# Kernel tuning notes

Measured on AMD Instinct MI355X. Metric: run time of the kernel, lower is better.

The kernel has to match this reference:

```python
import jax, jax.numpy as jnp
import numpy as np

N_NODES = 100000
N_EDGES = 800000
IN_FEAT = 128
HID = 128
OUT = 2


def setup_inputs() -> dict:
    key = jax.random.key(0)
    ks = jax.random.split(key, 8)
    h = jax.random.normal(ks[0], (N_NODES, IN_FEAT), dtype=jnp.float32)
    src = jax.random.randint(ks[1], (N_EDGES,), 0, N_NODES, dtype=jnp.int64)
    dst = jax.random.randint(ks[2], (N_EDGES,), 0, N_NODES, dtype=jnp.int64)
    # Linear weights stored as (fan_in, fan_out); scaled like torch's default init
    W1 = jax.random.normal(ks[3], (2 * IN_FEAT, HID), dtype=jnp.float32) / np.sqrt(2 * IN_FEAT)
    b1 = jnp.zeros((HID,), dtype=jnp.float32)
    W2 = jax.random.normal(ks[4], (HID, HID), dtype=jnp.float32) / np.sqrt(HID)
    b2 = jnp.zeros((HID,), dtype=jnp.float32)
    W3 = jax.random.normal(ks[5], (HID, OUT), dtype=jnp.float32) / np.sqrt(HID)
    b3 = jnp.zeros((OUT,), dtype=jnp.float32)
    return {"h": h, "src": src, "dst": dst,
            "W1": W1, "b1": b1, "W2": W2, "b2": b2, "W3": W3, "b3": b3}


def reference(h, src, dst, W1, b1, W2, b2, W3, b3):
    # Per-edge gather of endpoint features, concat, 3-layer MLP with ReLU
    h_u = h[src]                       # [E, F]
    h_v = h[dst]                       # [E, F]
    x = jnp.concatenate([h_u, h_v], axis=1)   # [E, 2F]
    x = jax.nn.relu(x @ W1 + b1)       # [E, HID]
    x = jax.nn.relu(x @ W2 + b2)       # [E, HID]
    score = x @ W3 + b3                # [E, OUT]
    return score
```

## Files before the change

kernel.cpp:

```cpp
#include <hip/hip_runtime.h>
#include <hip/hip_fp16.h>


typedef _Float16 half8 __attribute__((ext_vector_type(8)));
typedef _Float16 half4_t __attribute__((ext_vector_type(4)));
typedef float    f32x4 __attribute__((ext_vector_type(4)));

#define MFMA16(a, b, c) __builtin_amdgcn_mfma_f32_16x16x32_f16((a), (b), (c), 0, 0, 0)

#define N_NODES_C 100000
#define N_EDGES_C 800000

#define W1PF_OFF  0
#define W1QF_OFF  32768
#define W2F_OFF_N 65536
#define W3F_OFF_N 98304
#define P16_OFF   131072
#define TBL_HALVES (N_NODES_C * 128)
#define Q16_OFF   (P16_OFF + TBL_HALVES * 2)
#define WS_NEED_NEW ((size_t)Q16_OFF + (size_t)TBL_HALVES * 2)

#define ET 32
#define NT_E (N_EDGES_C / ET)
#define GRID_E 1024
#define NT_N ((N_NODES_C + 63) / 64)


__global__ void pack_w_new(const float* __restrict__ W1, const float* __restrict__ W2,
                           const float* __restrict__ W3, char* __restrict__ wsb) {
    int i = blockIdx.x * blockDim.x + threadIdx.x;
    _Float16* w1pf = (_Float16*)(wsb + W1PF_OFF);
    _Float16* w1qf = (_Float16*)(wsb + W1QF_OFF);
    _Float16* w2f  = (_Float16*)(wsb + W2F_OFF_N);
    _Float16* w3f  = (_Float16*)(wsb + W3F_OFF_N);
    if (i < 16384) {
        int j = i & 7, lane = (i >> 3) & 63, kk = (i >> 9) & 3, cm = i >> 11;
        int g = lane >> 4, rr = lane & 15;
        int k = 32 * kk + 8 * g + j, n = 16 * cm + rr;
        w1pf[i] = (_Float16)W1[k * 128 + n];
        w1qf[i] = (_Float16)W1[(k + 128) * 128 + n];
        w2f[i]  = (_Float16)W2[k * 128 + n];
    }
    if (i < 2048) {
        int j = i & 7, lane = (i >> 3) & 63, t = i >> 9;
        int g = lane >> 4, rr = lane & 15;
        int k = 32 * t + 4 * g + (j & 3) + 16 * (j >> 2);
        w3f[i] = (rr < 2) ? (_Float16)W3[k * 2 + rr] : (_Float16)0.0f;
    }
}

__global__ __launch_bounds__(512, 4) void pq_kernel(const float* __restrict__ h,
                                                    const float* __restrict__ b1,
                                                    char* __restrict__ wsb) {
    __shared__ float4 Htile[64 * 32];
    const int tid = threadIdx.x;
    const int w = tid >> 6, l = tid & 63, g = l >> 4, rr = l & 15;
    const int t = w >> 2, cmq = w & 3;
    const half8* wf = (const half8*)(wsb + (t ? W1QF_OFF : W1PF_OFF));
    half8 W1F[2][4];
#pragma unroll
    for (int cm = 0; cm < 2; ++cm)
#pragma unroll
        for (int kk = 0; kk < 4; ++kk)
            W1F[cm][kk] = wf[((2 * cmq + cm) * 4 + kk) * 64 + l];
    f32x4 b1v[2] = {{0.f, 0.f, 0.f, 0.f}, {0.f, 0.f, 0.f, 0.f}};
    if (t == 1) {
#pragma unroll
        for (int cm = 0; cm < 2; ++cm)
            b1v[cm] = *(const f32x4*)(b1 + 16 * (2 * cmq + cm) + 4 * g);
    }
    _Float16* tbl = (_Float16*)(wsb + (t ? Q16_OFF : P16_OFF));

    const int tile = blockIdx.x;
    const int slot = l & 31, rhalf = l >> 5;
    float4 sv[4];
    int rows[4];
#pragma unroll
    for (int i = 0; i < 4; ++i) {
        int row = 8 * w + 2 * i + rhalf;
        rows[i] = row;
        int node = tile * 64 + row;
        if (node > N_NODES_C - 1) node = N_NODES_C - 1;
        sv[i] = *(const float4*)(h + (size_t)node * 128 + slot * 4);
    }
#pragma unroll
    for (int i = 0; i < 4; ++i)
        Htile[rows[i] * 32 + (slot ^ (rows[i] & 15))] = sv[i];
    __syncthreads();

    f32x4 acc[2][4];
#pragma unroll
    for (int cm = 0; cm < 2; ++cm)
#pragma unroll
        for (int ce = 0; ce < 4; ++ce) acc[cm][ce] = f32x4{0.f, 0.f, 0.f, 0.f};
#pragma unroll
    for (int kk = 0; kk < 4; ++kk) {
#pragma unroll
        for (int ce = 0; ce < 4; ++ce) {
            int row = 16 * ce + rr;
            int s0 = kk * 8 + 2 * g;
            float4 fa = Htile[row * 32 + (s0 ^ rr)];
            float4 fb = Htile[row * 32 + ((s0 + 1) ^ rr)];
            half8 b;
            b[0] = (_Float16)fa.x; b[1] = (_Float16)fa.y;
            b[2] = (_Float16)fa.z; b[3] = (_Float16)fa.w;
            b[4] = (_Float16)fb.x; b[5] = (_Float16)fb.y;
            b[6] = (_Float16)fb.z; b[7] = (_Float16)fb.w;
            acc[0][ce] = MFMA16(W1F[0][kk], b, acc[0][ce]);
            acc[1][ce] = MFMA16(W1F[1][kk], b, acc[1][ce]);
        }
    }
#pragma unroll
    for (int cm = 0; cm < 2; ++cm)
#pragma unroll
        for (int ce = 0; ce < 4; ++ce) {
            int node = tile * 64 + 16 * ce + rr;
            if (node < N_NODES_C) {
                f32x4 v = acc[cm][ce] + b1v[cm];
                half4_t o;
                o[0] = (_Float16)v[0]; o[1] = (_Float16)v[1];
                o[2] = (_Float16)v[2]; o[3] = (_Float16)v[3];
                *(half4_t*)(tbl + (size_t)node * 128 + 16 * (2 * cmq + cm) + 4 * g) = o;
            }
        }
}


#define IDXLOAD(T, s0, s1, d0, d1)                            \
    {                                                          \
        int tt = (T); if (tt >= NT_E) tt = NT_E - 1;           \
        s0 = src[tt * ET + rr];  s1 = src[tt * ET + 16 + rr];  \
        d0 = dst[tt * ET + rr];  d1 = dst[tt * ET + 16 + rr];  \
    }

#define LOADSET(SP0, SP1, SQ0, SQ1, s0, s1, d0, d1)            \
    {                                                          \
        const half8* pr0 = P16 + (size_t)(s0) * 16 + g;        \
        const half8* pr1 = P16 + (size_t)(s1) * 16 + g;        \
        const half8* qr0 = Q16 + (size_t)(d0) * 16 + g;        \
        const half8* qr1 = Q16 + (size_t)(d1) * 16 + g;        \
        _Pragma("unroll")                                      \
        for (int kk = 0; kk < 4; ++kk) {                       \
            SP0[kk] = pr0[4 * kk];  SQ0[kk] = qr0[4 * kk];     \
            SP1[kk] = pr1[4 * kk];  SQ1[kk] = qr1[4 * kk];     \
        }                                                      \
    }

#define COMPUTE_STORE(SP0, SP1, SQ0, SQ1, TILE)                                 \
    {                                                                           \
        f32x4 acc[4][2];                                                        \
        _Pragma("unroll")                                                       \
        for (int cm = 0; cm < 4; ++cm) {                                        \
            acc[cm][0] = f32x4{0.f, 0.f, 0.f, 0.f};                             \
            acc[cm][1] = f32x4{0.f, 0.f, 0.f, 0.f};                             \
        }                                                                       \
        const half8 hz = {0, 0, 0, 0, 0, 0, 0, 0};                              \
        _Pragma("unroll")                                                       \
        for (int kk = 0; kk < 4; ++kk) {                                        \
            half8 bq0 = __builtin_elementwise_max(SP0[kk] + SQ0[kk], hz);       \
            half8 bq1 = __builtin_elementwise_max(SP1[kk] + SQ1[kk], hz);       \
            _Pragma("unroll")                                                   \
            for (int cm = 0; cm < 4; ++cm) {                                    \
                half8 wfr = W2lds[((4 * w + cm) * 4 + kk) * 64 + l];            \
                acc[cm][0] = MFMA16(wfr, bq0, acc[cm][0]);                      \
                acc[cm][1] = MFMA16(wfr, bq1, acc[cm][1]);                      \
            }                                                                   \
        }                                                                       \
        f32x4 D3[2] = {{0.f, 0.f, 0.f, 0.f}, {0.f, 0.f, 0.f, 0.f}};             \
        _Pragma("unroll")                                                       \
        for (int tl = 0; tl < 2; ++tl)                                          \
            _Pragma("unroll")                                                   \
            for (int ce = 0; ce < 2; ++ce) {                                    \
                half8 bf;                                                       \
                _Pragma("unroll")                                               \
                for (int j = 0; j < 8; ++j) {                                   \
                    const int cm = 2 * tl + (j >> 2), r = j & 3;                \
                    float v = acc[cm][ce][r] + (float)b2h[cm][r];               \
                    v = v > 0.f ? v : 0.f;                                      \
                    bf[j] = (_Float16)v;                                        \
                }                                                               \
                D3[ce] = MFMA16(W3F[tl], bf, D3[ce]);                           \
            }                                                                   \
        if (w == 1 && l < 16) {                                                 \
            part[par][0][rr] = make_float2(D3[0][0], D3[0][1]);                 \
            part[par][1][rr] = make_float2(D3[1][0], D3[1][1]);                 \
        }                                                                       \
        __syncthreads();                                                        \
        if (w == 0 && l < 16) {                                                 \
            _Pragma("unroll")                                                   \
            for (int ce = 0; ce < 2; ++ce) {                                    \
                float2 pp = part[par][ce][rr];                                  \
                float2 ov;                                                      \
                ov.x = D3[ce][0] + pp.x + b30;                                  \
                ov.y = D3[ce][1] + pp.y + b31;                                  \
                *(float2*)(out + (size_t)((TILE) * ET + 16 * ce + rr) * 2) = ov;\
            }                                                                   \
        }                                                                       \
        par ^= 1;                                                               \
    }

__global__ __launch_bounds__(128, 2) void edge_kernel(
    const int* __restrict__ src, const int* __restrict__ dst,
    const float* __restrict__ b2, const float* __restrict__ b3,
    const char* __restrict__ wsb, float* __restrict__ out) {
    __shared__ half8 W2lds[2048];
    __shared__ float2 part[2][2][16];
    const int tid = threadIdx.x;
    const int w = tid >> 6, l = tid & 63, g = l >> 4, rr = l & 15;
    const half8* w2fg = (const half8*)(wsb + W2F_OFF_N);
    const half8* w3f = (const half8*)(wsb + W3F_OFF_N);
    const half8* P16 = (const half8*)(wsb + P16_OFF);
    const half8* Q16 = (const half8*)(wsb + Q16_OFF);

#pragma unroll
    for (int i = 0; i < 16; ++i) W2lds[i * 128 + tid] = w2fg[i * 128 + tid];

    half8 W3F[2];
    W3F[0] = w3f[(2 * w) * 64 + l];
    W3F[1] = w3f[(2 * w + 1) * 64 + l];

    half4_t b2h[4];
#pragma unroll
    for (int cm = 0; cm < 4; ++cm) {
        f32x4 bv = *(const f32x4*)(b2 + 16 * (4 * w + cm) + 4 * g);
        b2h[cm][0] = (_Float16)bv[0]; b2h[cm][1] = (_Float16)bv[1];
        b2h[cm][2] = (_Float16)bv[2]; b2h[cm][3] = (_Float16)bv[3];
    }
    const float b30 = b3[0], b31 = b3[1];
    int par = 0;

    half8 PA0[4], PA1[4], QA0[4], QA1[4];
    half8 PB0[4], PB1[4], QB0[4], QB1[4];
    int ia0, ia1, ja0, ja1;
    int ib0, ib1, jb0, jb1;

    int tile = blockIdx.x;
    IDXLOAD(tile, ia0, ia1, ja0, ja1);
    LOADSET(PA0, PA1, QA0, QA1, ia0, ia1, ja0, ja1);
    IDXLOAD(tile + GRID_E, ib0, ib1, jb0, jb1);
    __syncthreads();

    for (;;) {
        LOADSET(PB0, PB1, QB0, QB1, ib0, ib1, jb0, jb1);
        __builtin_amdgcn_sched_barrier(0);
        IDXLOAD(tile + 2 * GRID_E, ia0, ia1, ja0, ja1);
        COMPUTE_STORE(PA0, PA1, QA0, QA1, tile);
        tile += GRID_E;
        if (tile >= NT_E) break;

        LOADSET(PA0, PA1, QA0, QA1, ia0, ia1, ja0, ja1);
        __builtin_amdgcn_sched_barrier(0);
        IDXLOAD(tile + 2 * GRID_E, ib0, ib1, jb0, jb1);
        COMPUTE_STORE(PB0, PB1, QB0, QB1, tile);
        tile += GRID_E;
        if (tile >= NT_E) break;
    }
}


#define NT_O   12500
#define GRID_O 512
#define OW1_OFF 0
#define OW2_OFF 65536
#define OW3_OFF 98304

__global__ void pack_w_old(const float* __restrict__ W1, const float* __restrict__ W2,
                           const float* __restrict__ W3, char* __restrict__ wsb) {
    int i = blockIdx.x * blockDim.x + threadIdx.x;
    _Float16* w1f = (_Float16*)(wsb + OW1_OFF);
    _Float16* w2f = (_Float16*)(wsb + OW2_OFF);
    _Float16* w3f = (_Float16*)(wsb + OW3_OFF);
    if (i < 32768) {
        int j = i & 7, lx = (i >> 3) & 63, kk = (i >> 9) & 7, t = i >> 12;
        int k = 32 * kk + 8 * (lx >> 4) + j, n = 16 * t + (lx & 15);
        w1f[i] = (_Float16)W1[k * 128 + n];
    }
    if (i < 16384) {
        int j = i & 7, lx = (i >> 3) & 63, kk = (i >> 9) & 3, t = i >> 11;
        int k = 32 * kk + 8 * (lx >> 4) + j, n = 16 * t + (lx & 15);
        w2f[i] = (_Float16)W2[k * 128 + n];
    }
    if (i < 2048) {
        int j = i & 7, lx = (i >> 3) & 63, kk = i >> 9;
        int k = 32 * kk + 8 * (lx >> 4) + j, n = lx & 15;
        w3f[i] = (n < 2) ? (_Float16)W3[k * 2 + n] : (_Float16)0.0f;
    }
}

__device__ inline half8 ldfrag_f32(const float* __restrict__ h, int idx, int kk, int g) {
    const float4* p = (const float4*)(h + (size_t)idx * 128 + (kk & 3) * 32 + g * 8);
    float4 a = p[0], b = p[1];
    half8 o;
    o[0] = (_Float16)a.x; o[1] = (_Float16)a.y; o[2] = (_Float16)a.z; o[3] = (_Float16)a.w;
    o[4] = (_Float16)b.x; o[5] = (_Float16)b.y; o[6] = (_Float16)b.z; o[7] = (_Float16)b.w;
    return o;
}

__global__ __launch_bounds__(256, 2) void edge_mlp_old(
    const float* __restrict__ h, const int* __restrict__ src, const int* __restrict__ dst,
    const float* __restrict__ b1, const float* __restrict__ b2, const float* __restrict__ b3,
    const char* __restrict__ wsb, float* __restrict__ out) {
    __shared__ half8 Xp [32 * 64];
    __shared__ half8 Y1p[16 * 64];
    __shared__ half8 Y2p[16 * 64];
    const int tid = threadIdx.x;
    const int w = tid >> 6, l = tid & 63;
    const int g = l >> 4, rr = l & 15;
    const int ghalf = rr >> 3, j7 = rr & 7;
    half8 W1F[2][8], W2F[2][4], W3F[4];
    {
        const half8* p1 = (const half8*)(wsb + OW1_OFF);
        const half8* p2 = (const half8*)(wsb + OW2_OFF);
        const half8* p3 = (const half8*)(wsb + OW3_OFF);
#pragma unroll
        for (int nt = 0; nt < 2; ++nt)
#pragma unroll
            for (int kk = 0; kk < 8; ++kk) W1F[nt][kk] = p1[((w * 2 + nt) * 8 + kk) * 64 + l];
#pragma unroll
        for (int nt = 0; nt < 2; ++nt)
#pragma unroll
            for (int kk = 0; kk < 4; ++kk) W2F[nt][kk] = p2[((w * 2 + nt) * 4 + kk) * 64 + l];
#pragma unroll
        for (int kk = 0; kk < 4; ++kk) W3F[kk] = p3[kk * 64 + l];
    }
    float b1r[2], b2r[2];
    b1r[0] = b1[w * 32 + rr];      b1r[1] = b1[w * 32 + 16 + rr];
    b2r[0] = b2[w * 32 + rr];      b2r[1] = b2[w * 32 + 16 + rr];
    const float b3r = (rr < 2) ? b3[rr] : 0.0f;
    _Float16* y1h = (_Float16*)Y1p;
    _Float16* y2h = (_Float16*)Y2p;
    int   idxn[8];
    half8 xt[8];
    int tile = blockIdx.x;
#pragma unroll
    for (int i = 0; i < 8; i++) {
        int bidx = w * 8 + i, kk = bidx >> 2;
        int e = ((i & 3) << 4) + rr;
        int id = (kk < 4 ? src : dst)[tile * 64 + e];
        xt[i] = ldfrag_f32(h, id, kk, g);
    }
#pragma unroll
    for (int i = 0; i < 8; i++) Xp[(w * 8 + i) * 64 + l] = xt[i];
    {
        int t1 = tile + GRID_O; if (t1 >= NT_O) t1 = NT_O - 1;
#pragma unroll
        for (int i = 0; i < 8; i++) {
            int bidx = w * 8 + i, kk = bidx >> 2;
            int e = ((i & 3) << 4) + rr;
            idxn[i] = (kk < 4 ? src : dst)[t1 * 64 + e];
        }
    }
    __syncthreads();
    for (; tile < NT_O; tile += GRID_O) {
        f32x4 acc1[4][2];
#pragma unroll
        for (int mt = 0; mt < 4; ++mt) {
            acc1[mt][0] = f32x4{0.f, 0.f, 0.f, 0.f};
            acc1[mt][1] = f32x4{0.f, 0.f, 0.f, 0.f};
        }
#pragma unroll
        for (int kk = 0; kk < 8; ++kk) {
            half8 a[4];
#pragma unroll
            for (int mt = 0; mt < 4; ++mt) a[mt] = Xp[(kk * 4 + mt) * 64 + l];
#pragma unroll
            for (int mt = 0; mt < 4; ++mt) {
                acc1[mt][0] = MFMA16(a[mt], W1F[0][kk], acc1[mt][0]);
                acc1[mt][1] = MFMA16(a[mt], W1F[1][kk], acc1[mt][1]);
            }
        }
#pragma unroll
        for (int i = 0; i < 8; i++) {
            int kk = (w * 8 + i) >> 2;
            xt[i] = ldfrag_f32(h, idxn[i], kk, g);
        }
        {
            int t2 = tile + 2 * GRID_O; if (t2 >= NT_O) t2 = NT_O - 1;
#pragma unroll
            for (int i = 0; i < 8; i++) {
                int bidx = w * 8 + i, kk = bidx >> 2;
                int e = ((i & 3) << 4) + rr;
                idxn[i] = (kk < 4 ? src : dst)[t2 * 64 + e];
            }
        }
#pragma unroll
        for (int mt = 0; mt < 4; ++mt)
#pragma unroll
            for (int nt = 0; nt < 2; ++nt) {
                float bb = b1r[nt];
#pragma unroll
                for (int r = 0; r < 4; ++r) {
                    float v = acc1[mt][nt][r] + bb;
                    v = v > 0.f ? v : 0.f;
                    y1h[(((w * 4 + mt) * 64 + 16 * (2 * nt + ghalf) + 4 * g + r) << 3) + j7] =
                        (_Float16)v;
                }
            }
        __syncthreads();
        f32x4 acc2[4][2];
#pragma unroll
        for (int mt = 0; mt < 4; ++mt) {
            acc2[mt][0] = f32x4{0.f, 0.f, 0.f, 0.f};
            acc2[mt][1] = f32x4{0.f, 0.f, 0.f, 0.f};
        }
#pragma unroll
        for (int kk = 0; kk < 4; ++kk) {
            half8 a[4];
#pragma unroll
            for (int mt = 0; mt < 4; ++mt) a[mt] = Y1p[(kk * 4 + mt) * 64 + l];
#pragma unroll
            for (int mt = 0; mt < 4; ++mt) {
                acc2[mt][0] = MFMA16(a[mt], W2F[0][kk], acc2[mt][0]);
                acc2[mt][1] = MFMA16(a[mt], W2F[1][kk], acc2[mt][1]);
            }
        }
#pragma unroll
        for (int mt = 0; mt < 4; ++mt)
#pragma unroll
            for (int nt = 0; nt < 2; ++nt) {
                float bb = b2r[nt];
#pragma unroll
                for (int r = 0; r < 4; ++r) {
                    float v = acc2[mt][nt][r] + bb;
                    v = v > 0.f ? v : 0.f;
                    y2h[(((w * 4 + mt) * 64 + 16 * (2 * nt + ghalf) + 4 * g + r) << 3) + j7] =
                        (_Float16)v;
                }
            }
        __syncthreads();
        f32x4 acc3 = {0.f, 0.f, 0.f, 0.f};
#pragma unroll
        for (int kk = 0; kk < 4; ++kk) {
            half8 a = Y2p[(kk * 4 + w) * 64 + l];
            acc3 = MFMA16(a, W3F[kk], acc3);
        }
        if (rr < 2) {
#pragma unroll
            for (int r = 0; r < 4; ++r) {
                int m = w * 16 + 4 * g + r;
                out[(tile * 64 + m) * 2 + rr] = acc3[r] + b3r;
            }
        }
#pragma unroll
        for (int i = 0; i < 8; i++) Xp[(w * 8 + i) * 64 + l] = xt[i];
        __syncthreads();
    }
}


extern "C" void kernel_launch(void* const* d_in, const int* in_sizes, int n_in,
                              void* d_out, int out_size, void* d_ws, size_t ws_size,
                              hipStream_t stream) {
    const float* h   = (const float*)d_in[0];
    const int*   src = (const int*)d_in[1];
    const int*   dst = (const int*)d_in[2];
    const float* W1  = (const float*)d_in[3];
    const float* b1  = (const float*)d_in[4];
    const float* W2  = (const float*)d_in[5];
    const float* b2  = (const float*)d_in[6];
    const float* W3  = (const float*)d_in[7];
    const float* b3  = (const float*)d_in[8];
    char*  wsb = (char*)d_ws;
    float* out = (float*)d_out;
    (void)in_sizes; (void)n_in; (void)out_size;

    if (ws_size >= WS_NEED_NEW) {
        pack_w_new<<<64, 256, 0, stream>>>(W1, W2, W3, wsb);
        pq_kernel<<<NT_N, 512, 0, stream>>>(h, b1, wsb);
        edge_kernel<<<GRID_E, 128, 0, stream>>>(src, dst, b2, b3, wsb, out);
    } else {
        pack_w_old<<<128, 256, 0, stream>>>(W1, W2, W3, wsb);
        edge_mlp_old<<<GRID_O, 256, 0, stream>>>(h, src, dst, b1, b2, b3, wsb, out);
    }
}
```

Baseline: 215.8 us.

## Give each wave full-width edge tiles and stage P/Q table stores through LDS

The edge kernel now has each wave compute all 128 hidden columns for its own 32-edge tile. The previous scheme split the columns across two waves and combined partial layer-3 sums through shared memory with a per-tile __syncthreads. Removing that barrier and exchange cuts inter-wave synchronisation, but each wave now needs more accumulator registers (16 f32x4 accumulators) and reads all of W2 from LDS, with 256-thread blocks and a grid of 512. The pq kernel also writes its half-precision P/Q results into a swizzled LDS tile first, then stores them as coalesced 16-byte rows, replacing scattered 8-byte global writes.

```diff
diff --git a/kernel.cpp b/kernel.cpp
--- a/kernel.cpp
+++ b/kernel.cpp
@@ -22,7 +22,8 @@
 
 #define ET 32
 #define NT_E (N_EDGES_C / ET)
-#define GRID_E 1024
+#define GRID_E 512
+#define WSTRIDE (GRID_E * 4)
 #define NT_N ((N_NODES_C + 63) / 64)
 
 
@@ -52,7 +53,8 @@
 __global__ __launch_bounds__(512, 4) void pq_kernel(const float* __restrict__ h,
                                                     const float* __restrict__ b1,
                                                     char* __restrict__ wsb) {
-    __shared__ float4 Htile[64 * 32];
+    __shared__ __align__(16) char SMEM[32768];
+    float4*   Htile = (float4*)SMEM;
     const int tid = threadIdx.x;
     const int w = tid >> 6, l = tid & 63, g = l >> 4, rr = l & 15;
     const int t = w >> 2, cmq = w & 3;
@@ -69,7 +71,6 @@
         for (int cm = 0; cm < 2; ++cm)
             b1v[cm] = *(const f32x4*)(b1 + 16 * (2 * cmq + cm) + 4 * g);
     }
-    _Float16* tbl = (_Float16*)(wsb + (t ? Q16_OFF : P16_OFF));
 
     const int tile = blockIdx.x;
     const int slot = l & 31, rhalf = l >> 5;
@@ -110,151 +111,168 @@
             acc[1][ce] = MFMA16(W1F[1][kk], b, acc[1][ce]);
         }
     }
+    __syncthreads();
+
 #pragma unroll
     for (int cm = 0; cm < 2; ++cm)
 #pragma unroll
         for (int ce = 0; ce < 4; ++ce) {
-            int node = tile * 64 + 16 * ce + rr;
-            if (node < N_NODES_C) {
-                f32x4 v = acc[cm][ce] + b1v[cm];
-                half4_t o;
-                o[0] = (_Float16)v[0]; o[1] = (_Float16)v[1];
-                o[2] = (_Float16)v[2]; o[3] = (_Float16)v[3];
-                *(half4_t*)(tbl + (size_t)node * 128 + 16 * (2 * cmq + cm) + 4 * g) = o;
-            }
-        }
-}
-
-
-#define IDXLOAD(T, s0, s1, d0, d1)                            \
-    {                                                          \
-        int tt = (T); if (tt >= NT_E) tt = NT_E - 1;           \
-        s0 = src[tt * ET + rr];  s1 = src[tt * ET + 16 + rr];  \
-        d0 = dst[tt * ET + rr];  d1 = dst[tt * ET + 16 + rr];  \
-    }
-
-#define LOADSET(SP0, SP1, SQ0, SQ1, s0, s1, d0, d1)            \
-    {                                                          \
-        const half8* pr0 = P16 + (size_t)(s0) * 16 + g;        \
-        const half8* pr1 = P16 + (size_t)(s1) * 16 + g;        \
-        const half8* qr0 = Q16 + (size_t)(d0) * 16 + g;        \
-        const half8* qr1 = Q16 + (size_t)(d1) * 16 + g;        \
-        _Pragma("unroll")                                      \
-        for (int kk = 0; kk < 4; ++kk) {                       \
-            SP0[kk] = pr0[4 * kk];  SQ0[kk] = qr0[4 * kk];     \
-            SP1[kk] = pr1[4 * kk];  SQ1[kk] = qr1[4 * kk];     \
-        }                                                      \
-    }
-
-#define COMPUTE_STORE(SP0, SP1, SQ0, SQ1, TILE)                                 \
+            int row = 16 * ce + rr;
+            f32x4 v = acc[cm][ce] + b1v[cm];
+            half4_t o;
+            o[0] = (_Float16)v[0]; o[1] = (_Float16)v[1];
+            o[2] = (_Float16)v[2]; o[3] = (_Float16)v[3];
+            int off = (32 * (2 * cmq + cm) + 8 * g) ^ ((row & 15) << 4);
+            *(half4_t*)(SMEM + t * 16384 + row * 256 + off) = o;
+        }
+    __syncthreads();
+
+    _Float16* Ptbl = (_Float16*)(wsb + P16_OFF);
+    _Float16* Qtbl = (_Float16*)(wsb + Q16_OFF);
+#pragma unroll
+    for (int p = 0; p < 4; ++p) {
+        int c = p * 512 + tid;
+        int tt = c >> 10, cc = c & 1023;
+        int row = cc >> 4, k = cc & 15;
+        int off = (16 * k) ^ ((row & 15) << 4);
+        float4 v4 = *(const float4*)(SMEM + tt * 16384 + row * 256 + off);
+        int node = tile * 64 + row;
+        if (node < N_NODES_C) {
+            _Float16* tb = tt ? Qtbl : Ptbl;
+            *(float4*)((char*)(tb + (size_t)node * 128) + 16 * k) = v4;
+        }
+    }
+}
+
+
+struct GSet { half8 P0[4], P1[4], Q0[4], Q1[4]; };
+
+__device__ __forceinline__ void load_set(GSet& s, const half8* __restrict__ P16,
+                                         const half8* __restrict__ Q16, int g,
+                                         int s0, int s1, int d0, int d1) {
+    const half8* pr0 = P16 + (size_t)s0 * 16 + g;
+    const half8* pr1 = P16 + (size_t)s1 * 16 + g;
+    const half8* qr0 = Q16 + (size_t)d0 * 16 + g;
+    const half8* qr1 = Q16 + (size_t)d1 * 16 + g;
+#pragma unroll
+    for (int kk = 0; kk < 4; ++kk) {
+        s.P0[kk] = pr0[4 * kk];  s.Q0[kk] = qr0[4 * kk];
+        s.P1[kk] = pr1[4 * kk];  s.Q1[kk] = qr1[4 * kk];
+    }
+}
+
+__global__ __launch_bounds__(256, 2) void edge_kernel(
+    const int* __restrict__ src, const int* __restrict__ dst,
+    const float* __restrict__ b2, const float* __restrict__ b3,
+    const char* __restrict__ wsb, float* __restrict__ out) {
+    __shared__ half8 W2lds[2048];
+    const int tid = threadIdx.x;
+    const int w = tid >> 6, l = tid & 63, g = l >> 4, rr = l & 15;
+    const half8* w2fg = (const half8*)(wsb + W2F_OFF_N);
+    const half8* w3f  = (const half8*)(wsb + W3F_OFF_N);
+    const half8* P16  = (const half8*)(wsb + P16_OFF);
+    const half8* Q16  = (const half8*)(wsb + Q16_OFF);
+
+#pragma unroll
+    for (int i = 0; i < 8; ++i) W2lds[i * 256 + tid] = w2fg[i * 256 + tid];
+
+    half8 W3F[4];
+#pragma unroll
+    for (int tt = 0; tt < 4; ++tt) W3F[tt] = w3f[tt * 64 + l];
+
+    half4_t b2h[8];
+#pragma unroll
+    for (int cm = 0; cm < 8; ++cm) {
+        f32x4 bv = *(const f32x4*)(b2 + 16 * cm + 4 * g);
+        b2h[cm][0] = (_Float16)bv[0]; b2h[cm][1] = (_Float16)bv[1];
+        b2h[cm][2] = (_Float16)bv[2]; b2h[cm][3] = (_Float16)bv[3];
+    }
+    const float b30 = b3[0], b31 = b3[1];
+
+    GSet A, B;
+    int ia0, ia1, ja0, ja1, ib0, ib1, jb0, jb1;
+
+    int t = blockIdx.x * 4 + w;
+    {
+        ia0 = src[t * ET + rr];  ia1 = src[t * ET + 16 + rr];
+        ja0 = dst[t * ET + rr];  ja1 = dst[t * ET + 16 + rr];
+    }
+    load_set(A, P16, Q16, g, ia0, ia1, ja0, ja1);
+    {
+        int tt = t + WSTRIDE; if (tt >= NT_E) tt = NT_E - 1;
+        ib0 = src[tt * ET + rr];  ib1 = src[tt * ET + 16 + rr];
+        jb0 = dst[tt * ET + rr];  jb1 = dst[tt * ET + 16 + rr];
+    }
+    __syncthreads();
+
+#define COMPUTE_STORE(S, T)                                                     \
     {                                                                           \
-        f32x4 acc[4][2];                                                        \
+        f32x4 acc[8][2];                                                        \
         _Pragma("unroll")                                                       \
-        for (int cm = 0; cm < 4; ++cm) {                                        \
+        for (int cm = 0; cm < 8; ++cm) {                                        \
             acc[cm][0] = f32x4{0.f, 0.f, 0.f, 0.f};                             \
             acc[cm][1] = f32x4{0.f, 0.f, 0.f, 0.f};                             \
         }                                                                       \
         const half8 hz = {0, 0, 0, 0, 0, 0, 0, 0};                              \
         _Pragma("unroll")                                                       \
         for (int kk = 0; kk < 4; ++kk) {                                        \
-            half8 bq0 = __builtin_elementwise_max(SP0[kk] + SQ0[kk], hz);       \
-            half8 bq1 = __builtin_elementwise_max(SP1[kk] + SQ1[kk], hz);       \
+            half8 bq0 = __builtin_elementwise_max(S.P0[kk] + S.Q0[kk], hz);     \
+            half8 bq1 = __builtin_elementwise_max(S.P1[kk] + S.Q1[kk], hz);     \
             _Pragma("unroll")                                                   \
-            for (int cm = 0; cm < 4; ++cm) {                                    \
-                half8 wfr = W2lds[((4 * w + cm) * 4 + kk) * 64 + l];            \
+            for (int cm = 0; cm < 8; ++cm) {                                    \
+                half8 wfr = W2lds[(cm * 4 + kk) * 64 + l];                      \
                 acc[cm][0] = MFMA16(wfr, bq0, acc[cm][0]);                      \
                 acc[cm][1] = MFMA16(wfr, bq1, acc[cm][1]);                      \
             }                                                                   \
         }                                                                       \
         f32x4 D3[2] = {{0.f, 0.f, 0.f, 0.f}, {0.f, 0.f, 0.f, 0.f}};             \
         _Pragma("unroll")                                                       \
-        for (int tl = 0; tl < 2; ++tl)                                          \
+        for (int tt = 0; tt < 4; ++tt)                                          \
             _Pragma("unroll")                                                   \
             for (int ce = 0; ce < 2; ++ce) {                                    \
                 half8 bf;                                                       \
                 _Pragma("unroll")                                               \
                 for (int j = 0; j < 8; ++j) {                                   \
-                    const int cm = 2 * tl + (j >> 2), r = j & 3;                \
+                    const int cm = 2 * tt + (j >> 2), r = j & 3;                \
                     float v = acc[cm][ce][r] + (float)b2h[cm][r];               \
                     v = v > 0.f ? v : 0.f;                                      \
                     bf[j] = (_Float16)v;                                        \
                 }                                                               \
-                D3[ce] = MFMA16(W3F[tl], bf, D3[ce]);                           \
+                D3[ce] = MFMA16(W3F[tt], bf, D3[ce]);                           \
             }                                                                   \
-        if (w == 1 && l < 16) {                                                 \
-            part[par][0][rr] = make_float2(D3[0][0], D3[0][1]);                 \
-            part[par][1][rr] = make_float2(D3[1][0], D3[1][1]);                 \
-        }                                                                       \
-        __syncthreads();                                                        \
-        if (w == 0 && l < 16) {                                                 \
+        if (g == 0) {                                                           \
             _Pragma("unroll")                                                   \
             for (int ce = 0; ce < 2; ++ce) {                                    \
-                float2 pp = part[par][ce][rr];                                  \
                 float2 ov;                                                      \
-                ov.x = D3[ce][0] + pp.x + b30;                                  \
-                ov.y = D3[ce][1] + pp.y + b31;                                  \
-                *(float2*)(out + (size_t)((TILE) * ET + 16 * ce + rr) * 2) = ov;\
+                ov.x = D3[ce][0] + b30;                                         \
+                ov.y = D3[ce][1] + b31;                                         \
+                *(float2*)(out + (size_t)((T) * ET + 16 * ce + rr) * 2) = ov;   \
             }                                                                   \
         }                                                                       \
-        par ^= 1;                                                               \
-    }
-
-__global__ __launch_bounds__(128, 2) void edge_kernel(
-    const int* __restrict__ src, const int* __restrict__ dst,
-    const float* __restrict__ b2, const float* __restrict__ b3,
-    const char* __restrict__ wsb, float* __restrict__ out) {
-    __shared__ half8 W2lds[2048];
-    __shared__ float2 part[2][2][16];
-    const int tid = threadIdx.x;
-    const int w = tid >> 6, l = tid & 63, g = l >> 4, rr = l & 15;
-    const half8* w2fg = (const half8*)(wsb + W2F_OFF_N);
-    const half8* w3f = (const half8*)(wsb + W3F_OFF_N);
-    const half8* P16 = (const half8*)(wsb + P16_OFF);
-    const half8* Q16 = (const half8*)(wsb + Q16_OFF);
-
-#pragma unroll
-    for (int i = 0; i < 16; ++i) W2lds[i * 128 + tid] = w2fg[i * 128 + tid];
-
-    half8 W3F[2];
-    W3F[0] = w3f[(2 * w) * 64 + l];
-    W3F[1] = w3f[(2 * w + 1) * 64 + l];
-
-    half4_t b2h[4];
-#pragma unroll
-    for (int cm = 0; cm < 4; ++cm) {
-        f32x4 bv = *(const f32x4*)(b2 + 16 * (4 * w + cm) + 4 * g);
-        b2h[cm][0] = (_Float16)bv[0]; b2h[cm][1] = (_Float16)bv[1];
-        b2h[cm][2] = (_Float16)bv[2]; b2h[cm][3] = (_Float16)bv[3];
-    }
-    const float b30 = b3[0], b31 = b3[1];
-    int par = 0;
-
-    half8 PA0[4], PA1[4], QA0[4], QA1[4];
-    half8 PB0[4], PB1[4], QB0[4], QB1[4];
-    int ia0, ia1, ja0, ja1;
-    int ib0, ib1, jb0, jb1;
-
-    int tile = blockIdx.x;
-    IDXLOAD(tile, ia0, ia1, ja0, ja1);
-    LOADSET(PA0, PA1, QA0, QA1, ia0, ia1, ja0, ja1);
-    IDXLOAD(tile + GRID_E, ib0, ib1, jb0, jb1);
-    __syncthreads();
+    }
 
     for (;;) {
-        LOADSET(PB0, PB1, QB0, QB1, ib0, ib1, jb0, jb1);
-        __builtin_amdgcn_sched_barrier(0);
-        IDXLOAD(tile + 2 * GRID_E, ia0, ia1, ja0, ja1);
-        COMPUTE_STORE(PA0, PA1, QA0, QA1, tile);
-        tile += GRID_E;
-        if (tile >= NT_E) break;
-
-        LOADSET(PA0, PA1, QA0, QA1, ia0, ia1, ja0, ja1);
-        __builtin_amdgcn_sched_barrier(0);
-        IDXLOAD(tile + 2 * GRID_E, ib0, ib1, jb0, jb1);
-        COMPUTE_STORE(PB0, PB1, QB0, QB1, tile);
-        tile += GRID_E;
-        if (tile >= NT_E) break;
-    }
+        load_set(B, P16, Q16, g, ib0, ib1, jb0, jb1);
+        {
+            int tt = t + 2 * WSTRIDE; if (tt >= NT_E) tt = NT_E - 1;
+            ia0 = src[tt * ET + rr];  ia1 = src[tt * ET + 16 + rr];
+            ja0 = dst[tt * ET + rr];  ja1 = dst[tt * ET + 16 + rr];
+        }
+        COMPUTE_STORE(A, t);
+        t += WSTRIDE;
+        if (t >= NT_E) break;
+
+        load_set(A, P16, Q16, g, ia0, ia1, ja0, ja1);
+        {
+            int tt = t + 2 * WSTRIDE; if (tt >= NT_E) tt = NT_E - 1;
+            ib0 = src[tt * ET + rr];  ib1 = src[tt * ET + 16 + rr];
+            jb0 = dst[tt * ET + rr];  jb1 = dst[tt * ET + 16 + rr];
+        }
+        COMPUTE_STORE(B, t);
+        t += WSTRIDE;
+        if (t >= NT_E) break;
+    }
+#undef COMPUTE_STORE
 }
 
 
@@ -467,7 +485,7 @@
     if (ws_size >= WS_NEED_NEW) {
         pack_w_new<<<64, 256, 0, stream>>>(W1, W2, W3, wsb);
         pq_kernel<<<NT_N, 512, 0, stream>>>(h, b1, wsb);
-        edge_kernel<<<GRID_E, 128, 0, stream>>>(src, dst, b2, b3, wsb, out);
+        edge_kernel<<<GRID_E, 256, 0, stream>>>(src, dst, b2, b3, wsb, out);
     } else {
         pack_w_old<<<128, 256, 0, stream>>>(W1, W2, W3, wsb);
         edge_mlp_old<<<GRID_O, 256, 0, stream>>>(h, src, dst, b1, b2, b3, wsb, out);
```

After: 244.7 us. 1.13x slower.
